# Kernel optimization log

Measured on AMD Instinct MI355X. Metric: run time of the kernel, lower is better.

## Reference

```python
import jax, jax.numpy as jnp
import numpy as np

B, H, W, C = 16, 256, 256, 64

def setup_inputs() -> dict:
    key = jax.random.key(0)
    k1, k2, k3 = jax.random.split(key, 3)
    x = jax.random.normal(k1, (B, H, W, C), dtype=jnp.float32)
    perm = jax.random.permutation(k2, B).astype(jnp.int32)
    alpha = jnp.clip(jax.random.uniform(k3, (B, 1, 1, 1), dtype=jnp.float32), 0.0, 0.95)
    return {"x": x, "perm": perm, "alpha": alpha}

def _wct(trg, src, alpha):
    # trg, src: (B, C, H, W)
    b, c, h, w = trg.shape
    hw = h * w
    trg_f = trg.reshape(b, c, hw)
    src_f = src.reshape(b, c, hw)
    src_mean = jnp.mean(src_f, axis=-1, keepdims=True)
    trg_mean = jnp.mean(trg_f, axis=-1, keepdims=True)
    src_red = src_f - src_mean
    trg_red = trg_f - trg_mean
    denom = jnp.float32(hw - 1)
    src_cov = jnp.matmul(src_red, src_red.transpose(0, 2, 1)) / denom  # (B,C,C)
    trg_cov = jnp.matmul(trg_red, trg_red.transpose(0, 2, 1)) / denom
    s_vals, s_vecs = jnp.linalg.eigh(src_cov)
    t_vals, t_vecs = jnp.linalg.eigh(trg_cov)
    s_sqrt = jnp.sqrt(jnp.maximum(s_vals, 1e-8))  # (B,C)
    t_sqrt = jnp.sqrt(jnp.maximum(t_vals, 1e-8))
    # W_trg = V diag(1/sqrt(lam)) V^T ; W_src_inv = V diag(sqrt(lam)) V^T
    W_trg = jnp.einsum('bij,bj,bkj->bik', t_vecs, 1.0 / t_sqrt, t_vecs)
    W_src_inv = jnp.einsum('bij,bj,bkj->bik', s_vecs, s_sqrt, s_vecs)
    trg_white = jnp.matmul(W_trg, trg_red)  # (B,C,HW)
    trg_tx = jnp.matmul(W_src_inv, trg_white) + src_mean
    trg_tx = trg_tx.reshape(b, c, h, w)
    return alpha * trg + (1.0 - alpha) * trg_tx

def reference(x, perm, alpha):
    t = jnp.transpose(x, (0, 3, 1, 2))  # (B,C,H,W)
    s = t[perm]
    out = _wct(t, s, alpha)
    return jnp.transpose(out, (0, 2, 3, 1))  # back to NHWC
```

## Files before the change

kernel.cpp:

```cpp
#include <hip/hip_runtime.h>

#define BATCH 16
#define CH    64
#define HW_PX 65536
#define NB2   128
#define PX2   512
#define TPX   64
#define NT2   (PX2 / TPX)
#define PARTIAL_STRIDE 4160

using bf16x8 = __attribute__((ext_vector_type(8))) short;
using f32x16 = __attribute__((ext_vector_type(16))) float;
using f32x4  = __attribute__((ext_vector_type(4))) float;

__device__ inline unsigned short bf16_rne(float f) {
    unsigned int u = __builtin_bit_cast(unsigned int, f);
    u += 0x7FFFu + ((u >> 16) & 1u);
    return (unsigned short)(u >> 16);
}
__device__ inline float bf16_f32(unsigned short s) {
    unsigned int u = ((unsigned int)s) << 16;
    return __builtin_bit_cast(float, u);
}
__device__ inline int sw_idx(int row, int col) {
    return row * 64 + ((((col >> 3) ^ (row & 7)) << 3) | (col & 7));
}
__device__ inline bf16x8 ld_frag8(const short* m, int row, int o) {
    return *(const bf16x8*)&m[row * 64 + ((o ^ (row & 7)) << 3)];
}
__device__ inline void mm_quad_hilo(f32x16& acc,
        const short* Ah, const short* Al,
        const short* Bh, const short* Bl,
        int ra, int rb, int lane) {
    #pragma unroll
    for (int kc = 0; kc < 4; ++kc) {
        int o = kc * 2 + (lane >> 5);
        bf16x8 ah = ld_frag8(Ah, ra, o);
        bf16x8 al = ld_frag8(Al, ra, o);
        bf16x8 bh = ld_frag8(Bh, rb, o);
        bf16x8 bl = ld_frag8(Bl, rb, o);
        acc = __builtin_amdgcn_mfma_f32_32x32x16_bf16(ah, bh, acc, 0, 0, 0);
        acc = __builtin_amdgcn_mfma_f32_32x32x16_bf16(ah, bl, acc, 0, 0, 0);
        acc = __builtin_amdgcn_mfma_f32_32x32x16_bf16(al, bh, acc, 0, 0, 0);
    }
}
__device__ inline void wb_hilo(short* Mh, short* Ml, const f32x16& v,
                               int r, int cq, int lane, float scale, float diag) {
    #pragma unroll
    for (int reg = 0; reg < 16; ++reg) {
        int row = 32 * r + (reg & 3) + 8 * (reg >> 2) + 4 * (lane >> 5);
        int col = 32 * cq + (lane & 31);
        float f = v[reg] * scale + ((row == col) ? diag : 0.0f);
        unsigned short hi = bf16_rne(f);
        float lo = f - bf16_f32(hi);
        int idx = sw_idx(row, col);
        Mh[idx] = (short)hi;
        Ml[idx] = (short)bf16_rne(lo);
    }
}

template<int NB1T>
__global__ __launch_bounds__(256, 6) void pass1_cov(const float* __restrict__ x,
                                                    float* __restrict__ partial) {
    constexpr int PX1T = HW_PX / NB1T;
    constexpr int NT1T = PX1T / 64;
    const int blk = blockIdx.x;
    const int b = blk / NB1T;
    const int chunk = blk % NB1T;
    const size_t base = (size_t)b * HW_PX * CH + (size_t)chunk * PX1T * CH;
    const int t = threadIdx.x;
    const int lane = t & 63;
    const int wave = t >> 6;
    const int r = wave >> 1, cq = wave & 1;
    const int s_ch = t & 63;
    const int s_og = t >> 6;

    __shared__ __align__(16) short xs[2][4096];
    __shared__ float fsum[256];

    f32x16 acc;
    #pragma unroll
    for (int i = 0; i < 16; ++i) acc[i] = 0.0f;
    float csum = 0.0f;

    {
        const size_t tb = base;
        #pragma unroll
        for (int p = 0; p < 2; ++p) {
            const int o = s_og + 4 * p;
            bf16x8 w;
            #pragma unroll
            for (int j = 0; j < 8; ++j) {
                float v = x[tb + (size_t)(o * 8 + j) * CH + s_ch];
                csum += v;
                w[j] = (short)bf16_rne(v);
            }
            *(bf16x8*)&xs[0][s_ch * 64 + ((o ^ (s_ch & 7)) << 3)] = w;
        }
    }
    __syncthreads();

    const int ra = 32 * r + (lane & 31);
    const int rb = 32 * cq + (lane & 31);

    for (int tile = 0; tile < NT1T; ++tile) {
        const int cur = tile & 1;
        if (tile + 1 < NT1T) {
            const size_t tb = base + (size_t)(tile + 1) * 64 * CH;
            const int nb = cur ^ 1;
            #pragma unroll
            for (int p = 0; p < 2; ++p) {
                const int o = s_og + 4 * p;
                bf16x8 w;
                #pragma unroll
                for (int j = 0; j < 8; ++j) {
                    float v = x[tb + (size_t)(o * 8 + j) * CH + s_ch];
                    csum += v;
                    w[j] = (short)bf16_rne(v);
                }
                *(bf16x8*)&xs[nb][s_ch * 64 + ((o ^ (s_ch & 7)) << 3)] = w;
            }
        }
        #pragma unroll
        for (int kc = 0; kc < 4; ++kc) {
            const int o = kc * 2 + (lane >> 5);
            bf16x8 af = *(const bf16x8*)&xs[cur][ra * 64 + ((o ^ (ra & 7)) << 3)];
            bf16x8 bg = *(const bf16x8*)&xs[cur][rb * 64 + ((o ^ (rb & 7)) << 3)];
            acc = __builtin_amdgcn_mfma_f32_32x32x16_bf16(af, bg, acc, 0, 0, 0);
        }
        __syncthreads();
    }

    float* myp = partial + (size_t)blk * PARTIAL_STRIDE;
    #pragma unroll
    for (int reg = 0; reg < 16; ++reg) {
        int row = 32 * r + (reg & 3) + 8 * (reg >> 2) + 4 * (lane >> 5);
        int col = 32 * cq + (lane & 31);
        myp[row * 64 + col] = acc[reg];
    }
    fsum[t] = csum;
    __syncthreads();
    if (t < 64) {
        myp[4096 + t] = fsum[t] + fsum[t + 64] + fsum[t + 128] + fsum[t + 192];
    }
}

template<int NB1T>
__global__ __launch_bounds__(256) void reduce_cov(const float* __restrict__ partial,
                                                  float* __restrict__ meanv,
                                                  float* __restrict__ cov) {
    const int b = blockIdx.x >> 4;
    const int s = blockIdx.x & 15;
    const int t = threadIdx.x;
    __shared__ float msh[64];
    if (t < 64) {
        float su = 0.0f;
        for (int k = 0; k < NB1T; ++k)
            su += partial[(size_t)(b * NB1T + k) * PARTIAL_STRIDE + 4096 + t];
        float m = su / (float)HW_PX;
        msh[t] = m;
        if (s == 0) meanv[b * 64 + t] = m;
    }
    __syncthreads();
    const float invn = 1.0f / (float)(HW_PX - 1);
    const int e = s * 256 + t;
    float su = 0.0f;
    for (int k = 0; k < NB1T; ++k)
        su += partial[(size_t)(b * NB1T + k) * PARTIAL_STRIDE + e];
    const int i = e >> 6, j = e & 63;
    cov[b * 4096 + e] = (su - (float)HW_PX * msh[i] * msh[j]) * invn;
}

__global__ __launch_bounds__(256) void ns_sqrt(
        const float* __restrict__ cov,
        float* __restrict__ Ym, float* __restrict__ Zm) {
    const int b = blockIdx.x;
    const int t = threadIdx.x;
    const int lane = t & 63;
    const int wave = t >> 6;
    const int r = wave >> 1, cq = wave & 1;
    __shared__ __align__(16) short Yh[4096], Yl[4096], Zh[4096], Zl[4096], Ph[4096], Pl[4096];
    __shared__ float csh;
    float* Cf = (float*)Ph;

    for (int e = t; e < 4096; e += 256)
        Cf[e] = cov[b * 4096 + e];
    __syncthreads();
    if (t == 0) {
        float tr = 0.0f;
        for (int i = 0; i < 64; ++i) tr += Cf[i * 64 + i];
        csh = 64.0f / tr;
    }
    __syncthreads();
    const float invc = csh;
    for (int e = t; e < 4096; e += 256) {
        int row = e >> 6, col = e & 63;
        float y = Cf[e] * invc;
        unsigned short hi = bf16_rne(y);
        float lo = y - bf16_f32(hi);
        int idx = sw_idx(row, col);
        Yh[idx] = (short)hi; Yl[idx] = (short)bf16_rne(lo);
        Zh[idx] = (row == col) ? (short)0x3F80 : (short)0;
        Zl[idx] = 0;
    }
    __syncthreads();

    const int ra = 32 * r + (lane & 31);
    const int rb = 32 * cq + (lane & 31);
    for (int it = 0; it < 5; ++it) {
        f32x16 tacc;
        #pragma unroll
        for (int i = 0; i < 16; ++i) tacc[i] = 0.0f;
        mm_quad_hilo(tacc, Zh, Zl, Yh, Yl, ra, rb, lane);
        wb_hilo(Ph, Pl, tacc, r, cq, lane, -0.5f, 1.5f);
        __syncthreads();
        f32x16 ya, za;
        #pragma unroll
        for (int i = 0; i < 16; ++i) { ya[i] = 0.0f; za[i] = 0.0f; }
        mm_quad_hilo(ya, Yh, Yl, Ph, Pl, ra, rb, lane);
        mm_quad_hilo(za, Ph, Pl, Zh, Zl, ra, rb, lane);
        __syncthreads();
        wb_hilo(Yh, Yl, ya, r, cq, lane, 1.0f, 0.0f);
        wb_hilo(Zh, Zl, za, r, cq, lane, 1.0f, 0.0f);
        __syncthreads();
    }

    const float c = 1.0f / invc;
    const float sc = sqrtf(c);
    const float isc = 1.0f / sc;
    float* yo = Ym + b * 4096;
    float* zo = Zm + b * 4096;
    for (int e = t; e < 4096; e += 256) {
        int row = e >> 6, col = e & 63;
        int idx = sw_idx(row, col);
        yo[e] = (bf16_f32((unsigned short)Yh[idx]) + bf16_f32((unsigned short)Yl[idx])) * sc;
        zo[e] = (bf16_f32((unsigned short)Zh[idx]) + bf16_f32((unsigned short)Zl[idx])) * isc;
    }
}

__global__ __launch_bounds__(256) void combine(
        const float* __restrict__ Ym, const float* __restrict__ Zm,
        const float* __restrict__ meanv,
        const int* __restrict__ perm, const float* __restrict__ alpha,
        float* __restrict__ Amat, float* __restrict__ evec) {
    const int b = blockIdx.x;
    const int t = threadIdx.x;
    const int lane = t & 63;
    const int wave = t >> 6;
    const int r = wave >> 1, cq = wave & 1;
    const int sb = perm[b];
    __shared__ __align__(16) short Yh[4096], Yl[4096], Zh[4096], Zl[4096];
    __shared__ float Mf[64 * 66];
    const float* yg = Ym + sb * 4096;
    const float* zg = Zm + b * 4096;
    for (int e = t; e < 4096; e += 256) {
        int row = e >> 6, col = e & 63;
        int idx = sw_idx(row, col);
        float y = yg[e];
        unsigned short hy = bf16_rne(y);
        Yh[idx] = (short)hy; Yl[idx] = (short)bf16_rne(y - bf16_f32(hy));
        float z = zg[e];
        unsigned short hz = bf16_rne(z);
        Zh[idx] = (short)hz; Zl[idx] = (short)bf16_rne(z - bf16_f32(hz));
    }
    __syncthreads();
    f32x16 acc;
    #pragma unroll
    for (int i = 0; i < 16; ++i) acc[i] = 0.0f;
    const int ra = 32 * r + (lane & 31);
    const int rb = 32 * cq + (lane & 31);
    mm_quad_hilo(acc, Yh, Yl, Zh, Zl, ra, rb, lane);
    const float al = alpha[b];
    float* Ab = Amat + b * 4096;
    #pragma unroll
    for (int reg = 0; reg < 16; ++reg) {
        int row = 32 * r + (reg & 3) + 8 * (reg >> 2) + 4 * (lane >> 5);
        int col = 32 * cq + (lane & 31);
        float mv = acc[reg];
        Mf[row * 66 + col] = mv;
        Ab[row * 64 + col] = (1.0f - al) * mv + ((row == col) ? al : 0.0f);
    }
    __syncthreads();
    if (t < 64) {
        const float* mt = meanv + b * 64;
        const float* ms = meanv + sb * 64;
        float s = 0.0f;
        for (int k = 0; k < 64; ++k) s += Mf[t * 66 + k] * mt[k];
        evec[b * 64 + t] = (1.0f - al) * (ms[t] - s);
    }
}

__global__ __launch_bounds__(256, 8) void pass2_apply(const float* __restrict__ x,
                                                      const float* __restrict__ Amat,
                                                      const float* __restrict__ evec,
                                                      float* __restrict__ out) {
    const int blk = blockIdx.x;
    const int b = blk / NB2;
    const int chunk = blk % NB2;
    const int t = threadIdx.x;
    const int lane = t & 63;
    const int wave = t >> 6;
    const int pr = wave >> 1;
    const int c2 = wave & 1;
    const size_t base = (size_t)b * HW_PX * CH + (size_t)chunk * PX2 * CH;

    __shared__ __align__(16) short xs[2][TPX * 64];

    const int ch_out = 32 * c2 + (lane & 31);
    const float* Ab = Amat + b * 4096;
    bf16x8 bfrag[4];
    #pragma unroll
    for (int kc = 0; kc < 4; ++kc) {
        bf16x8 f;
        #pragma unroll
        for (int j = 0; j < 8; ++j)
            f[j] = (short)bf16_rne(Ab[ch_out * 64 + kc * 16 + (lane >> 5) * 8 + j]);
        bfrag[kc] = f;
    }
    const float ebias = evec[b * 64 + ch_out];

    const int oct = t & 7;
    const int spx = t >> 3;
    auto stage = [&](int buf, int tile) {
        const size_t tb = base + (size_t)tile * TPX * CH;
        #pragma unroll
        for (int p = 0; p < 2; ++p) {
            const int px = p * 32 + spx;
            const float* src = &x[tb + (size_t)px * CH + oct * 8];
            f32x4 v0 = *(const f32x4*)src;
            f32x4 v1 = *(const f32x4*)(src + 4);
            bf16x8 w;
            #pragma unroll
            for (int j = 0; j < 4; ++j) w[j] = (short)bf16_rne(v0[j]);
            #pragma unroll
            for (int j = 0; j < 4; ++j) w[4 + j] = (short)bf16_rne(v1[j]);
            *(bf16x8*)&xs[buf][px * 64 + ((oct ^ (px & 7)) << 3)] = w;
        }
    };

    stage(0, 0);
    __syncthreads();

    const int ra = 32 * pr + (lane & 31);
    #pragma unroll 1
    for (int tile = 0; tile < NT2; ++tile) {
        const int cur = tile & 1;
        if (tile + 1 < NT2) stage(cur ^ 1, tile + 1);

        f32x16 acc;
        #pragma unroll
        for (int i = 0; i < 16; ++i) acc[i] = ebias;
        #pragma unroll
        for (int kc = 0; kc < 4; ++kc) {
            bf16x8 ah = ld_frag8(&xs[cur][0], ra, kc * 2 + (lane >> 5));
            acc = __builtin_amdgcn_mfma_f32_32x32x16_bf16(ah, bfrag[kc], acc, 0, 0, 0);
        }

        const size_t tb = base + (size_t)tile * TPX * CH;
        #pragma unroll
        for (int reg = 0; reg < 16; ++reg) {
            const int px = 32 * pr + (reg & 3) + 8 * (reg >> 2) + 4 * (lane >> 5);
            out[tb + (size_t)px * CH + ch_out] = acc[reg];
        }
        __syncthreads();
    }
}

extern "C" void kernel_launch(void* const* d_in, const int* in_sizes, int n_in,
                              void* d_out, int out_size, void* d_ws, size_t ws_size,
                              hipStream_t stream) {
    (void)in_sizes; (void)n_in; (void)out_size;
    const float* x     = (const float*)d_in[0];
    const int*   perm  = (const int*)d_in[1];
    const float* alpha = (const float*)d_in[2];
    float* out = (float*)d_out;

    const size_t rest_elems = (size_t)BATCH * 4096
                            + (size_t)BATCH * 64
                            + (size_t)BATCH * 4096 * 3
                            + (size_t)BATCH * 64;
    auto need = [&](int nb) {
        return ((size_t)BATCH * nb * PARTIAL_STRIDE + rest_elems) * sizeof(float);
    };
    const int nb1 = (ws_size >= need(128)) ? 128 : (ws_size >= need(64)) ? 64 : 32;

    float* ws      = (float*)d_ws;
    float* partial = ws;
    float* cov     = partial + (size_t)BATCH * nb1 * PARTIAL_STRIDE;
    float* meanv   = cov + BATCH * 4096;
    float* Ym      = meanv + BATCH * 64;
    float* Zm      = Ym + BATCH * 4096;
    float* Am      = Zm + BATCH * 4096;
    float* ev      = Am + BATCH * 4096;

    if (nb1 == 128) {
        pass1_cov<128> <<<BATCH * 128, 256, 0, stream>>>(x, partial);
        reduce_cov<128><<<BATCH * 16,  256, 0, stream>>>(partial, meanv, cov);
    } else if (nb1 == 64) {
        pass1_cov<64>  <<<BATCH * 64,  256, 0, stream>>>(x, partial);
        reduce_cov<64> <<<BATCH * 16,  256, 0, stream>>>(partial, meanv, cov);
    } else {
        pass1_cov<32>  <<<BATCH * 32,  256, 0, stream>>>(x, partial);
        reduce_cov<32> <<<BATCH * 16,  256, 0, stream>>>(partial, meanv, cov);
    }
    ns_sqrt    <<<BATCH,       256, 0, stream>>>(cov, Ym, Zm);
    combine    <<<BATCH,       256, 0, stream>>>(Ym, Zm, meanv, perm, alpha, Am, ev);
    pass2_apply<<<BATCH * NB2, 256, 0, stream>>>(x, Am, ev, out);
}
```

Before: 545.5 us.

## Fuse WCT pipeline into one cooperative persistent kernel with grid syncs

Replaces the five separate launches (covariance partials, reduction, Newton-Schulz sqrt, combine, apply) with one cooperative kernel of 768 blocks that separates the phases with grid syncs. The apply phase walks its tiles in reverse so the most recently read part of x may still be in cache, and the output stores are nontemporal. This removes launch gaps and inter-kernel idle time. In exchange, 752 blocks sit idle during the two single-block-per-batch phases, grid syncs add their own overhead, and the old multi-kernel path remains as a fallback if a cooperative launch is not possible.

```diff
diff --git a/kernel.cpp b/kernel.cpp
--- a/kernel.cpp
+++ b/kernel.cpp
@@ -1,13 +1,18 @@
 #include <hip/hip_runtime.h>
+#include <hip/hip_cooperative_groups.h>
+namespace cg = cooperative_groups;
 
 #define BATCH 16
 #define CH    64
 #define HW_PX 65536
-#define NB2   128
-#define PX2   512
-#define TPX   64
-#define NT2   (PX2 / TPX)
+#define GRIDF 768
+#define BPB   (GRIDF / BATCH)
+#define TPB   1024
 #define PARTIAL_STRIDE 4160
+#define NB2 128
+#define PX2 512
+#define TPX 64
+#define NT2 (PX2 / TPX)
 
 using bf16x8 = __attribute__((ext_vector_type(8))) short;
 using f32x16 = __attribute__((ext_vector_type(16))) float;
@@ -56,6 +61,282 @@
         int idx = sw_idx(row, col);
         Mh[idx] = (short)hi;
         Ml[idx] = (short)bf16_rne(lo);
+    }
+}
+
+#define SM_BYTES 50176
+
+__global__ __launch_bounds__(256, 3) void wct_fused(
+        const float* __restrict__ x, const int* __restrict__ perm,
+        const float* __restrict__ alpha, float* __restrict__ out,
+        float* __restrict__ partial, float* __restrict__ cov,
+        float* __restrict__ meanv, float* __restrict__ Ym,
+        float* __restrict__ Zm, float* __restrict__ Am,
+        float* __restrict__ ev)
+{
+    cg::grid_group gg = cg::this_grid();
+    __shared__ __align__(16) unsigned char smem[SM_BYTES];
+    const int w = blockIdx.x;
+    const int t = threadIdx.x;
+    const int lane = t & 63;
+    const int wave = t >> 6;
+    const int b = w / BPB, j = w % BPB;
+
+    {
+        short* xs = (short*)smem;
+        float* fsum = (float*)(smem + 16384);
+        const int r = wave >> 1, cq = wave & 1;
+        const int t0 = (j * TPB) / BPB, t1 = ((j + 1) * TPB) / BPB;
+        const size_t xb = (size_t)b * HW_PX * CH;
+        const int s_ch = t & 63, s_og = t >> 6;
+        f32x16 acc;
+        #pragma unroll
+        for (int i = 0; i < 16; ++i) acc[i] = 0.0f;
+        float csum = 0.0f;
+        auto stage1 = [&](int buf, int tile) {
+            const size_t tb = xb + (size_t)tile * 64 * CH;
+            #pragma unroll
+            for (int p = 0; p < 2; ++p) {
+                const int o = s_og + 4 * p;
+                bf16x8 wv;
+                #pragma unroll
+                for (int jj = 0; jj < 8; ++jj) {
+                    float v = x[tb + (size_t)(o * 8 + jj) * CH + s_ch];
+                    csum += v;
+                    wv[jj] = (short)bf16_rne(v);
+                }
+                *(bf16x8*)&xs[buf * 4096 + s_ch * 64 + ((o ^ (s_ch & 7)) << 3)] = wv;
+            }
+        };
+        stage1(0, t0);
+        __syncthreads();
+        const int ra = 32 * r + (lane & 31);
+        const int rb = 32 * cq + (lane & 31);
+        const int nt = t1 - t0;
+        for (int k = 0; k < nt; ++k) {
+            const int cur = k & 1;
+            if (k + 1 < nt) stage1(cur ^ 1, t0 + k + 1);
+            #pragma unroll
+            for (int kc = 0; kc < 4; ++kc) {
+                const int o = kc * 2 + (lane >> 5);
+                bf16x8 af = ld_frag8(xs + cur * 4096, ra, o);
+                bf16x8 bg = ld_frag8(xs + cur * 4096, rb, o);
+                acc = __builtin_amdgcn_mfma_f32_32x32x16_bf16(af, bg, acc, 0, 0, 0);
+            }
+            __syncthreads();
+        }
+        float* myp = partial + (size_t)w * PARTIAL_STRIDE;
+        #pragma unroll
+        for (int reg = 0; reg < 16; ++reg) {
+            int row = 32 * r + (reg & 3) + 8 * (reg >> 2) + 4 * (lane >> 5);
+            int col = 32 * cq + (lane & 31);
+            myp[row * 64 + col] = acc[reg];
+        }
+        fsum[t] = csum;
+        __syncthreads();
+        if (t < 64)
+            myp[4096 + t] = fsum[t] + fsum[t + 64] + fsum[t + 128] + fsum[t + 192];
+    }
+    __threadfence();
+    gg.sync();
+
+    {
+        float* msh = (float*)(smem + 49664);
+        if (t < 64) {
+            float su = 0.0f;
+            for (int k = 0; k < BPB; ++k)
+                su += partial[(size_t)(b * BPB + k) * PARTIAL_STRIDE + 4096 + t];
+            float m = su / (float)HW_PX;
+            msh[t] = m;
+            if (j == 0) meanv[b * 64 + t] = m;
+        }
+        __syncthreads();
+        const float invn = 1.0f / (float)(HW_PX - 1);
+        const int e0 = (j * 4096) / BPB, e1 = ((j + 1) * 4096) / BPB;
+        for (int e = e0 + t; e < e1; e += 256) {
+            float su = 0.0f;
+            for (int k = 0; k < BPB; ++k)
+                su += partial[(size_t)(b * BPB + k) * PARTIAL_STRIDE + e];
+            cov[b * 4096 + e] = (su - (float)HW_PX * msh[e >> 6] * msh[e & 63]) * invn;
+        }
+    }
+    __threadfence();
+    gg.sync();
+
+    if (w < BATCH) {
+        short* Yh = (short*)smem;
+        short* Yl = (short*)(smem + 8192);
+        short* Zh = (short*)(smem + 16384);
+        short* Zl = (short*)(smem + 24576);
+        short* Ph = (short*)(smem + 32768);
+        short* Pl = (short*)(smem + 40960);
+        float* csh = (float*)(smem + 49920);
+        float* Cf = (float*)Ph;
+        const int r = wave >> 1, cq = wave & 1;
+
+        for (int e = t; e < 4096; e += 256)
+            Cf[e] = cov[w * 4096 + e];
+        __syncthreads();
+        if (t == 0) {
+            float tr = 0.0f;
+            for (int i = 0; i < 64; ++i) tr += Cf[i * 64 + i];
+            csh[0] = 64.0f / tr;
+        }
+        __syncthreads();
+        const float invc = csh[0];
+        for (int e = t; e < 4096; e += 256) {
+            int row = e >> 6, col = e & 63;
+            float y = Cf[e] * invc;
+            unsigned short hi = bf16_rne(y);
+            float lo = y - bf16_f32(hi);
+            int idx = sw_idx(row, col);
+            Yh[idx] = (short)hi; Yl[idx] = (short)bf16_rne(lo);
+            Zh[idx] = (row == col) ? (short)0x3F80 : (short)0;
+            Zl[idx] = 0;
+        }
+        __syncthreads();
+        const int ra = 32 * r + (lane & 31);
+        const int rb = 32 * cq + (lane & 31);
+        for (int it = 0; it < 5; ++it) {
+            f32x16 tacc;
+            #pragma unroll
+            for (int i = 0; i < 16; ++i) tacc[i] = 0.0f;
+            mm_quad_hilo(tacc, Zh, Zl, Yh, Yl, ra, rb, lane);
+            wb_hilo(Ph, Pl, tacc, r, cq, lane, -0.5f, 1.5f);
+            __syncthreads();
+            f32x16 ya, za;
+            #pragma unroll
+            for (int i = 0; i < 16; ++i) { ya[i] = 0.0f; za[i] = 0.0f; }
+            mm_quad_hilo(ya, Yh, Yl, Ph, Pl, ra, rb, lane);
+            mm_quad_hilo(za, Ph, Pl, Zh, Zl, ra, rb, lane);
+            __syncthreads();
+            wb_hilo(Yh, Yl, ya, r, cq, lane, 1.0f, 0.0f);
+            wb_hilo(Zh, Zl, za, r, cq, lane, 1.0f, 0.0f);
+            __syncthreads();
+        }
+        const float c = 1.0f / invc;
+        const float sc = sqrtf(c);
+        const float isc = 1.0f / sc;
+        float* yo = Ym + w * 4096;
+        float* zo = Zm + w * 4096;
+        for (int e = t; e < 4096; e += 256) {
+            int row = e >> 6, col = e & 63;
+            int idx = sw_idx(row, col);
+            yo[e] = (bf16_f32((unsigned short)Yh[idx]) + bf16_f32((unsigned short)Yl[idx])) * sc;
+            zo[e] = (bf16_f32((unsigned short)Zh[idx]) + bf16_f32((unsigned short)Zl[idx])) * isc;
+        }
+    }
+    __threadfence();
+    gg.sync();
+
+    if (w < BATCH) {
+        short* Yh = (short*)smem;
+        short* Yl = (short*)(smem + 8192);
+        short* Zh = (short*)(smem + 16384);
+        short* Zl = (short*)(smem + 24576);
+        float* Mf = (float*)(smem + 32768);
+        const int r = wave >> 1, cq = wave & 1;
+        const int sb = perm[w];
+        const float* yg = Ym + sb * 4096;
+        const float* zg = Zm + w * 4096;
+        for (int e = t; e < 4096; e += 256) {
+            int row = e >> 6, col = e & 63;
+            int idx = sw_idx(row, col);
+            float y = yg[e];
+            unsigned short hy = bf16_rne(y);
+            Yh[idx] = (short)hy; Yl[idx] = (short)bf16_rne(y - bf16_f32(hy));
+            float z = zg[e];
+            unsigned short hz = bf16_rne(z);
+            Zh[idx] = (short)hz; Zl[idx] = (short)bf16_rne(z - bf16_f32(hz));
+        }
+        __syncthreads();
+        f32x16 acc;
+        #pragma unroll
+        for (int i = 0; i < 16; ++i) acc[i] = 0.0f;
+        const int ra = 32 * r + (lane & 31);
+        const int rb = 32 * cq + (lane & 31);
+        mm_quad_hilo(acc, Yh, Yl, Zh, Zl, ra, rb, lane);
+        const float al = alpha[w];
+        float* Ab = Am + w * 4096;
+        #pragma unroll
+        for (int reg = 0; reg < 16; ++reg) {
+            int row = 32 * r + (reg & 3) + 8 * (reg >> 2) + 4 * (lane >> 5);
+            int col = 32 * cq + (lane & 31);
+            float mv = acc[reg];
+            Mf[row * 66 + col] = mv;
+            Ab[row * 64 + col] = (1.0f - al) * mv + ((row == col) ? al : 0.0f);
+        }
+        __syncthreads();
+        if (t < 64) {
+            const float* mt = meanv + w * 64;
+            const float* ms = meanv + sb * 64;
+            float s = 0.0f;
+            for (int k = 0; k < 64; ++k) s += Mf[t * 66 + k] * mt[k];
+            ev[w * 64 + t] = (1.0f - al) * (ms[t] - s);
+        }
+    }
+    __threadfence();
+    gg.sync();
+
+    {
+        short* xs = (short*)smem;
+        const int pr = wave >> 1, c2 = wave & 1;
+        const int t0 = (j * TPB) / BPB, t1 = ((j + 1) * TPB) / BPB;
+        const size_t xb = (size_t)b * HW_PX * CH;
+        const int ch_out = 32 * c2 + (lane & 31);
+        const float* Ab = Am + b * 4096;
+        bf16x8 bfrag[4];
+        #pragma unroll
+        for (int kc = 0; kc < 4; ++kc) {
+            bf16x8 f;
+            #pragma unroll
+            for (int jj = 0; jj < 8; ++jj)
+                f[jj] = (short)bf16_rne(Ab[ch_out * 64 + kc * 16 + (lane >> 5) * 8 + jj]);
+            bfrag[kc] = f;
+        }
+        const float ebias = ev[b * 64 + ch_out];
+        const int oct = t & 7, spx = t >> 3;
+        auto stage2 = [&](int buf, int tile) {
+            const size_t tb = xb + (size_t)tile * 64 * CH;
+            #pragma unroll
+            for (int p = 0; p < 2; ++p) {
+                const int px = p * 32 + spx;
+                const float* src = &x[tb + (size_t)px * CH + oct * 8];
+                f32x4 v0 = *(const f32x4*)src;
+                f32x4 v1 = *(const f32x4*)(src + 4);
+                bf16x8 wv;
+                #pragma unroll
+                for (int jj = 0; jj < 4; ++jj) wv[jj] = (short)bf16_rne(v0[jj]);
+                #pragma unroll
+                for (int jj = 0; jj < 4; ++jj) wv[4 + jj] = (short)bf16_rne(v1[jj]);
+                *(bf16x8*)&xs[buf * 4096 + px * 64 + ((oct ^ (px & 7)) << 3)] = wv;
+            }
+        };
+        stage2(0, t1 - 1);
+        __syncthreads();
+        const int ra = 32 * pr + (lane & 31);
+        const int nt = t1 - t0;
+        #pragma unroll 1
+        for (int k = 0; k < nt; ++k) {
+            const int tile = t1 - 1 - k;
+            const int cur = k & 1;
+            if (k + 1 < nt) stage2(cur ^ 1, tile - 1);
+            f32x16 acc;
+            #pragma unroll
+            for (int i = 0; i < 16; ++i) acc[i] = ebias;
+            #pragma unroll
+            for (int kc = 0; kc < 4; ++kc) {
+                bf16x8 ah = ld_frag8(xs + cur * 4096, ra, kc * 2 + (lane >> 5));
+                acc = __builtin_amdgcn_mfma_f32_32x32x16_bf16(ah, bfrag[kc], acc, 0, 0, 0);
+            }
+            const size_t tb = xb + (size_t)tile * 64 * CH;
+            #pragma unroll
+            for (int reg = 0; reg < 16; ++reg) {
+                const int px = 32 * pr + (reg & 3) + 8 * (reg >> 2) + 4 * (lane >> 5);
+                __builtin_nontemporal_store(acc[reg], &out[tb + (size_t)px * CH + ch_out]);
+            }
+            __syncthreads();
+        }
     }
 }
 
@@ -74,35 +355,30 @@
     const int r = wave >> 1, cq = wave & 1;
     const int s_ch = t & 63;
     const int s_og = t >> 6;
-
     __shared__ __align__(16) short xs[2][4096];
     __shared__ float fsum[256];
-
     f32x16 acc;
     #pragma unroll
     for (int i = 0; i < 16; ++i) acc[i] = 0.0f;
     float csum = 0.0f;
-
     {
         const size_t tb = base;
         #pragma unroll
         for (int p = 0; p < 2; ++p) {
             const int o = s_og + 4 * p;
-            bf16x8 w;
-            #pragma unroll
-            for (int j = 0; j < 8; ++j) {
-                float v = x[tb + (size_t)(o * 8 + j) * CH + s_ch];
+            bf16x8 wv;
+            #pragma unroll
+            for (int jj = 0; jj < 8; ++jj) {
+                float v = x[tb + (size_t)(o * 8 + jj) * CH + s_ch];
                 csum += v;
-                w[j] = (short)bf16_rne(v);
+                wv[jj] = (short)bf16_rne(v);
             }
-            *(bf16x8*)&xs[0][s_ch * 64 + ((o ^ (s_ch & 7)) << 3)] = w;
-        }
-    }
-    __syncthreads();
-
+            *(bf16x8*)&xs[0][s_ch * 64 + ((o ^ (s_ch & 7)) << 3)] = wv;
+        }
+    }
+    __syncthreads();
     const int ra = 32 * r + (lane & 31);
     const int rb = 32 * cq + (lane & 31);
-
     for (int tile = 0; tile < NT1T; ++tile) {
         const int cur = tile & 1;
         if (tile + 1 < NT1T) {
@@ -111,14 +387,14 @@
             #pragma unroll
             for (int p = 0; p < 2; ++p) {
                 const int o = s_og + 4 * p;
-                bf16x8 w;
+                bf16x8 wv;
                 #pragma unroll
-                for (int j = 0; j < 8; ++j) {
-                    float v = x[tb + (size_t)(o * 8 + j) * CH + s_ch];
+                for (int jj = 0; jj < 8; ++jj) {
+                    float v = x[tb + (size_t)(o * 8 + jj) * CH + s_ch];
                     csum += v;
-                    w[j] = (short)bf16_rne(v);
+                    wv[jj] = (short)bf16_rne(v);
                 }
-                *(bf16x8*)&xs[nb][s_ch * 64 + ((o ^ (s_ch & 7)) << 3)] = w;
+                *(bf16x8*)&xs[nb][s_ch * 64 + ((o ^ (s_ch & 7)) << 3)] = wv;
             }
         }
         #pragma unroll
@@ -130,7 +406,6 @@
         }
         __syncthreads();
     }
-
     float* myp = partial + (size_t)blk * PARTIAL_STRIDE;
     #pragma unroll
     for (int reg = 0; reg < 16; ++reg) {
@@ -140,9 +415,8 @@
     }
     fsum[t] = csum;
     __syncthreads();
-    if (t < 64) {
+    if (t < 64)
         myp[4096 + t] = fsum[t] + fsum[t + 64] + fsum[t + 128] + fsum[t + 192];
-    }
 }
 
 template<int NB1T>
@@ -167,8 +441,8 @@
     float su = 0.0f;
     for (int k = 0; k < NB1T; ++k)
         su += partial[(size_t)(b * NB1T + k) * PARTIAL_STRIDE + e];
-    const int i = e >> 6, j = e & 63;
-    cov[b * 4096 + e] = (su - (float)HW_PX * msh[i] * msh[j]) * invn;
+    const int i = e >> 6, jj = e & 63;
+    cov[b * 4096 + e] = (su - (float)HW_PX * msh[i] * msh[jj]) * invn;
 }
 
 __global__ __launch_bounds__(256) void ns_sqrt(
@@ -182,7 +456,6 @@
     __shared__ __align__(16) short Yh[4096], Yl[4096], Zh[4096], Zl[4096], Ph[4096], Pl[4096];
     __shared__ float csh;
     float* Cf = (float*)Ph;
-
     for (int e = t; e < 4096; e += 256)
         Cf[e] = cov[b * 4096 + e];
     __syncthreads();
@@ -204,7 +477,6 @@
         Zl[idx] = 0;
     }
     __syncthreads();
-
     const int ra = 32 * r + (lane & 31);
     const int rb = 32 * cq + (lane & 31);
     for (int it = 0; it < 5; ++it) {
@@ -224,7 +496,6 @@
         wb_hilo(Zh, Zl, za, r, cq, lane, 1.0f, 0.0f);
         __syncthreads();
     }
-
     const float c = 1.0f / invc;
     const float sc = sqrtf(c);
     const float isc = 1.0f / sc;
@@ -303,9 +574,7 @@
     const int pr = wave >> 1;
     const int c2 = wave & 1;
     const size_t base = (size_t)b * HW_PX * CH + (size_t)chunk * PX2 * CH;
-
     __shared__ __align__(16) short xs[2][TPX * 64];
-
     const int ch_out = 32 * c2 + (lane & 31);
     const float* Ab = Amat + b * 4096;
     bf16x8 bfrag[4];
@@ -313,12 +582,11 @@
     for (int kc = 0; kc < 4; ++kc) {
         bf16x8 f;
         #pragma unroll
-        for (int j = 0; j < 8; ++j)
-            f[j] = (short)bf16_rne(Ab[ch_out * 64 + kc * 16 + (lane >> 5) * 8 + j]);
+        for (int jj = 0; jj < 8; ++jj)
+            f[jj] = (short)bf16_rne(Ab[ch_out * 64 + kc * 16 + (lane >> 5) * 8 + jj]);
         bfrag[kc] = f;
     }
     const float ebias = evec[b * 64 + ch_out];
-
     const int oct = t & 7;
     const int spx = t >> 3;
     auto stage = [&](int buf, int tile) {
@@ -329,24 +597,21 @@
             const float* src = &x[tb + (size_t)px * CH + oct * 8];
             f32x4 v0 = *(const f32x4*)src;
             f32x4 v1 = *(const f32x4*)(src + 4);
-            bf16x8 w;
-            #pragma unroll
-            for (int j = 0; j < 4; ++j) w[j] = (short)bf16_rne(v0[j]);
-            #pragma unroll
-            for (int j = 0; j < 4; ++j) w[4 + j] = (short)bf16_rne(v1[j]);
-            *(bf16x8*)&xs[buf][px * 64 + ((oct ^ (px & 7)) << 3)] = w;
+            bf16x8 wv;
+            #pragma unroll
+            for (int jj = 0; jj < 4; ++jj) wv[jj] = (short)bf16_rne(v0[jj]);
+            #pragma unroll
+            for (int jj = 0; jj < 4; ++jj) wv[4 + jj] = (short)bf16_rne(v1[jj]);
+            *(bf16x8*)&xs[buf][px * 64 + ((oct ^ (px & 7)) << 3)] = wv;
         }
     };
-
     stage(0, 0);
     __syncthreads();
-
     const int ra = 32 * pr + (lane & 31);
     #pragma unroll 1
     for (int tile = 0; tile < NT2; ++tile) {
         const int cur = tile & 1;
         if (tile + 1 < NT2) stage(cur ^ 1, tile + 1);
-
         f32x16 acc;
         #pragma unroll
         for (int i = 0; i < 16; ++i) acc[i] = ebias;
@@ -355,7 +620,6 @@
             bf16x8 ah = ld_frag8(&xs[cur][0], ra, kc * 2 + (lane >> 5));
             acc = __builtin_amdgcn_mfma_f32_32x32x16_bf16(ah, bfrag[kc], acc, 0, 0, 0);
         }
-
         const size_t tb = base + (size_t)tile * TPX * CH;
         #pragma unroll
         for (int reg = 0; reg < 16; ++reg) {
@@ -374,6 +638,35 @@
     const int*   perm  = (const int*)d_in[1];
     const float* alpha = (const float*)d_in[2];
     float* out = (float*)d_out;
+    float* ws  = (float*)d_ws;
+
+    {
+        float* partial = ws;
+        float* cov   = partial + (size_t)GRIDF * PARTIAL_STRIDE;
+        float* meanv = cov + BATCH * 4096;
+        float* Ym    = meanv + BATCH * 64;
+        float* Zm    = Ym + BATCH * 4096;
+        float* Am    = Zm + BATCH * 4096;
+        float* ev    = Am + BATCH * 4096;
+        const size_t need_f = ((size_t)GRIDF * PARTIAL_STRIDE
+                             + (size_t)BATCH * (4096 * 4 + 128)) * sizeof(float);
+        int dev = 0;
+        hipGetDevice(&dev);
+        int coop = 0;
+        hipDeviceGetAttribute(&coop, hipDeviceAttributeCooperativeLaunch, dev);
+        int ncu = 0;
+        hipDeviceGetAttribute(&ncu, hipDeviceAttributeMultiprocessorCount, dev);
+        int maxb = 0;
+        hipOccupancyMaxActiveBlocksPerMultiprocessor(&maxb, wct_fused, 256, 0);
+        if (coop && ws_size >= need_f && maxb >= 1 && (size_t)maxb * (size_t)ncu >= GRIDF) {
+            void* args[] = { (void*)&x, (void*)&perm, (void*)&alpha, (void*)&out,
+                             (void*)&partial, (void*)&cov, (void*)&meanv,
+                             (void*)&Ym, (void*)&Zm, (void*)&Am, (void*)&ev };
+            hipError_t e = hipLaunchCooperativeKernel((const void*)wct_fused,
+                               dim3(GRIDF), dim3(256), args, 0, stream);
+            if (e == hipSuccess) return;
+        }
+    }
 
     const size_t rest_elems = (size_t)BATCH * 4096
                             + (size_t)BATCH * 64
@@ -383,8 +676,6 @@
         return ((size_t)BATCH * nb * PARTIAL_STRIDE + rest_elems) * sizeof(float);
     };
     const int nb1 = (ws_size >= need(128)) ? 128 : (ws_size >= need(64)) ? 64 : 32;
-
-    float* ws      = (float*)d_ws;
     float* partial = ws;
     float* cov     = partial + (size_t)BATCH * nb1 * PARTIAL_STRIDE;
     float* meanv   = cov + BATCH * 4096;
@@ -392,7 +683,6 @@
     float* Zm      = Ym + BATCH * 4096;
     float* Am      = Zm + BATCH * 4096;
     float* ev      = Am + BATCH * 4096;
-
     if (nb1 == 128) {
         pass1_cov<128> <<<BATCH * 128, 256, 0, stream>>>(x, partial);
         reduce_cov<128><<<BATCH * 16,  256, 0, stream>>>(partial, meanv, cov);
```

After: 548.1 us. No clear change (+0.5%).
